# Optimization experiments

Hardware: AMD Instinct MI355X
Metric: run time of the kernel (lower is better)

The kernel has to match this reference:

```python
import jax, jax.numpy as jnp
import numpy as np

B, Cin, Cout, K, H, W = 16, 32, 32, 3, 256, 256
EMB = 256  # layer_pos_embedding_size == condition_size == 256


def setup_inputs() -> dict:
    key = jax.random.key(0)
    ks = jax.random.split(key, 7)
    return {
        "x": jax.random.normal(ks[0], (B, Cin, H, W), jnp.float32),
        "condition": jax.random.normal(ks[1], (B, EMB), jnp.float32),
        "layer_pos_embedding": jax.random.normal(ks[2], (B, EMB), jnp.float32),
        # base conv weight, stored [Cin, Cout, K, K] as in the torch module
        "weights": jax.random.normal(ks[3], (Cin, Cout, K, K), jnp.float32) * 0.05,
        "bias": jax.random.normal(ks[4], (Cout,), jnp.float32) * 0.05,
        # weightAdapt: Linear(2*EMB -> Cin); biasAdapt: Linear(2*EMB -> Cout)
        "wa_w": jax.random.normal(ks[5], (Cin, 2 * EMB), jnp.float32) * 0.04,
        "wa_b": jnp.zeros((Cin,), jnp.float32),
        "ba_w": jax.random.normal(ks[6], (Cout, 2 * EMB), jnp.float32) * 0.04,
        "ba_b": jnp.zeros((Cout,), jnp.float32),
    }


def reference(x, condition, layer_pos_embedding, weights, bias, wa_w, wa_b, ba_w, ba_b):
    # i = cat([condition, layer_pos_embedding])  -> [B, 2*EMB]
    i = jnp.concatenate([condition, layer_pos_embedding], axis=-1)
    wadapt = i @ wa_w.T + wa_b   # [B, Cin]  per-sample input-channel modulation
    badapt = i @ ba_w.T + ba_b   # [B, Cout] per-sample bias modulation
    # per-sample OIHW kernel: (weights [Cin,Cout,K,K] * wadapt[b,Cin,1,1,1]) rearranged
    kern = jnp.einsum('iokl,bi->boikl', weights, wadapt)  # [B, Cout, Cin, K, K]

    def conv1(xi, ki):
        # xi: [Cin,H,W], ki: [Cout,Cin,K,K] -> [Cout,H,W], padding='same', stride 1
        return jax.lax.conv_general_dilated(
            xi[None], ki, window_strides=(1, 1), padding='SAME',
            dimension_numbers=('NCHW', 'OIHW', 'NCHW'))[0]

    o = jax.vmap(conv1)(x, kern)  # [B, Cout, H, W] (== groups=batch grouped conv)
    # modulated bias add per (batch, out_channel)
    return o + (bias[None, :] * badapt)[:, :, None, None]
```

## Files before the change

### kernel.cpp

```cpp
#include <hip/hip_runtime.h>


#define B_    16
#define CIN   32
#define COUT  32
#define H_    256
#define W_    256
#define EMB2  512

#define XPX       66
#define PXS       32
#define ROWS_     (XPX*PXS)
#define NSLOT     8

using short8  = __attribute__((ext_vector_type(8))) short;
using float4v = __attribute__((ext_vector_type(4))) float;

__device__ __forceinline__ unsigned short f2bf(float f) {
    unsigned u = __builtin_bit_cast(unsigned, f);
    u += 0x7FFFu + ((u >> 16) & 1u);
    return (unsigned short)(u >> 16);
}
__device__ __forceinline__ unsigned pk2(float a, float b) {
    return (unsigned)f2bf(a) | ((unsigned)f2bf(b) << 16);
}

__global__ __launch_bounds__(256) void adapt_kernel(
    const float* __restrict__ cond, const float* __restrict__ lpe,
    const float* __restrict__ wa_w, const float* __restrict__ wa_b,
    const float* __restrict__ ba_w, const float* __restrict__ ba_b,
    const float* __restrict__ bias, float* __restrict__ ws)
{
    __shared__ float iv[EMB2];
    __shared__ float partial[64][4];
    const int b = blockIdx.x;
    const int t = threadIdx.x;

    iv[t]       = cond[b*256 + t];
    iv[t + 256] = lpe[b*256 + t];
    __syncthreads();

    const int out  = t & 63;
    const int part = t >> 6;
    const float* row = (out < 32) ? (wa_w + out*EMB2) : (ba_w + (out-32)*EMB2);
    float s = 0.f;
    #pragma unroll 8
    for (int j = part*128; j < part*128 + 128; ++j) s += iv[j] * row[j];
    partial[out][part] = s;
    __syncthreads();

    if (t < 64) {
        float v = partial[t][0] + partial[t][1] + partial[t][2] + partial[t][3];
        if (t < 32) ws[b*32 + t] = v + wa_b[t];
        else {
            int o = t - 32;
            ws[512 + b*32 + o] = bias[o] * (v + ba_b[o]);
        }
    }
}

__global__ __launch_bounds__(256, 2) void conv_kernel(
    const float* __restrict__ x, const float* __restrict__ weights,
    const float* __restrict__ ws, float* __restrict__ out)
{
    __shared__ unsigned short xbuf[NSLOT * ROWS_];
    __shared__ unsigned short wbuf[9 * COUT * PXS];

    const int tid    = threadIdx.x;
    const int lane   = tid & 63;
    const int w      = tid >> 6;
    const int ln15   = lane & 15;
    const int kg     = lane >> 4;
    const int xstrip = blockIdx.x * 64;
    const int ystrip = blockIdx.y * 32;
    const int b      = blockIdx.z;

    for (int idx = tid; idx < CIN*COUT*9; idx += 256) {
        int i   = idx / 288;
        int rem = idx - i*288;
        int o   = rem / 9;
        int tap = rem - o*9;
        float v = weights[idx] * ws[b*32 + i];
        wbuf[tap*1024 + o*32 + i] = f2bf(v);
    }

    auto stage = [&](int r0, int nrows) {
        const int total = nrows * XPX * 4;
        for (int idx = tid; idx < total; idx += 256) {
            int p  = idx % XPX;
            int t2 = idx / XPX;
            int g  = t2 & 3;
            int rr = t2 >> 2;
            int r  = r0 + rr;
            int gy = ystrip + r;
            int gx = xstrip + p - 1;
            int slot = (r + 1) & 7;
            unsigned dst = slot*ROWS_ + p*PXS + ((g ^ ((p >> 1) & 3)) * 8);
            uint4 pk;
            if (((unsigned)gy < 256u) & ((unsigned)gx < 256u)) {
                const float* src = x + (((size_t)(b*CIN + g*8) << 16) + (gy << 8) + gx);
                float f0 = src[0*65536], f1 = src[1*65536];
                float f2 = src[2*65536], f3 = src[3*65536];
                float f4 = src[4*65536], f5 = src[5*65536];
                float f6 = src[6*65536], f7 = src[7*65536];
                pk.x = pk2(f0, f1); pk.y = pk2(f2, f3);
                pk.z = pk2(f4, f5); pk.w = pk2(f6, f7);
            } else {
                pk = uint4{0u, 0u, 0u, 0u};
            }
            *(uint4*)&xbuf[dst] = pk;
        }
    };

    stage(-1, 6);
    __syncthreads();

    short8 wA[9][2];
    #pragma unroll
    for (int tap = 0; tap < 9; ++tap)
        #pragma unroll
        for (int ot = 0; ot < 2; ++ot) {
            int o = ot*16 + ln15;
            wA[tap][ot] = *(const short8*)&wbuf[tap*1024 + o*32 + kg*8];
        }

    float bm[2][4];
    #pragma unroll
    for (int ot = 0; ot < 2; ++ot)
        #pragma unroll
        for (int r = 0; r < 4; ++r)
            bm[ot][r] = ws[512 + b*32 + ot*16 + kg*4 + r];

    for (int t = 0; t < 8; ++t) {
        if (t > 0) {
            stage(4*t + 1, 4);
            __syncthreads();
        }

        const int orow = 4*t + w;
        const int gy   = ystrip + orow;

        float4v acc[4][2];
        #pragma unroll
        for (int c = 0; c < 4; ++c) {
            acc[c][0] = float4v{0.f, 0.f, 0.f, 0.f};
            acc[c][1] = float4v{0.f, 0.f, 0.f, 0.f};
        }

        #pragma unroll
        for (int dy = 0; dy < 3; ++dy) {
            const int rowbase = ((orow + dy) & 7) * ROWS_;
            #pragma unroll
            for (int dx = 0; dx < 3; ++dx) {
                const int tap = dy*3 + dx;
                #pragma unroll
                for (int c = 0; c < 4; ++c) {
                    int p = c*16 + dx + ln15;
                    int a = rowbase + p*PXS + ((kg ^ ((p >> 1) & 3)) * 8);
                    short8 xf = *(const short8*)&xbuf[a];
                    acc[c][0] = __builtin_amdgcn_mfma_f32_16x16x32_bf16(
                                    wA[tap][0], xf, acc[c][0], 0, 0, 0);
                    acc[c][1] = __builtin_amdgcn_mfma_f32_16x16x32_bf16(
                                    wA[tap][1], xf, acc[c][1], 0, 0, 0);
                }
            }
        }
        __syncthreads();

        #pragma unroll
        for (int c = 0; c < 4; ++c) {
            const int xcol = xstrip + c*16 + ln15;
            #pragma unroll
            for (int ot = 0; ot < 2; ++ot) {
                const int obase = ot*16 + kg*4;
                #pragma unroll
                for (int r = 0; r < 4; ++r) {
                    out[(((size_t)(b*COUT + obase + r) << 8) + gy << 8) + xcol] =
                        acc[c][ot][r] + bm[ot][r];
                }
            }
        }
    }
}

extern "C" void kernel_launch(void* const* d_in, const int* in_sizes, int n_in,
                              void* d_out, int out_size, void* d_ws, size_t ws_size,
                              hipStream_t stream) {
    const float* x       = (const float*)d_in[0];
    const float* cond    = (const float*)d_in[1];
    const float* lpe     = (const float*)d_in[2];
    const float* weights = (const float*)d_in[3];
    const float* bias    = (const float*)d_in[4];
    const float* wa_w    = (const float*)d_in[5];
    const float* wa_b    = (const float*)d_in[6];
    const float* ba_w    = (const float*)d_in[7];
    const float* ba_b    = (const float*)d_in[8];
    float* outp = (float*)d_out;
    float* ws   = (float*)d_ws;

    adapt_kernel<<<dim3(B_), dim3(256), 0, stream>>>(
        cond, lpe, wa_w, wa_b, ba_w, ba_b, bias, ws);

    conv_kernel<<<dim3(W_/64, H_/32, B_), dim3(256), 0, stream>>>(
        x, weights, ws, outp);
}
```

Measured before the change: 276.1 us.

## Use 512-thread blocks with register-prefetched row ring and LDS-resident weights

Doubles the conv block to 8 waves, each computing one output row per iteration, and widens the LDS row ring to 10 slots. The next 8 input rows are loaded into registers before compute and written to LDS after it, so global-load latency overlaps the MFMA work. Halo columns are staged separately. Per-tap weight fragments now live in LDS in a lane-ordered layout and are reloaded per tap instead of kept in registers. The tighter launch bound (512 threads, 4 blocks) caps VGPRs, so the 32-float prefetch buffer plus accumulators may spill.

Measured after the change: 311.6 us. 12.9% more time.

```diff
diff --git a/kernel.cpp b/kernel.cpp
--- a/kernel.cpp
+++ b/kernel.cpp
@@ -8,10 +8,10 @@
 #define W_    256
 #define EMB2  512
 
-#define XPX       66
-#define PXS       32
-#define ROWS_     (XPX*PXS)
-#define NSLOT     8
+#define XPX   66
+#define PXS   32
+#define ROWS_ (XPX*PXS)
+#define NSLOT 10
 
 using short8  = __attribute__((ext_vector_type(8))) short;
 using float4v = __attribute__((ext_vector_type(4))) float;
@@ -59,12 +59,12 @@
     }
 }
 
-__global__ __launch_bounds__(256, 2) void conv_kernel(
+__global__ __launch_bounds__(512, 4) void conv_kernel(
     const float* __restrict__ x, const float* __restrict__ weights,
     const float* __restrict__ ws, float* __restrict__ out)
 {
-    __shared__ unsigned short xbuf[NSLOT * ROWS_];
-    __shared__ unsigned short wbuf[9 * COUT * PXS];
+    __shared__ __align__(16) unsigned short xbuf[NSLOT * ROWS_];
+    __shared__ __align__(16) unsigned short wbuf[9 * 2 * 64 * 8];
 
     const int tid    = threadIdx.x;
     const int lane   = tid & 63;
@@ -75,54 +75,51 @@
     const int ystrip = blockIdx.y * 32;
     const int b      = blockIdx.z;
 
-    for (int idx = tid; idx < CIN*COUT*9; idx += 256) {
+    for (int idx = tid; idx < CIN*COUT*9; idx += 512) {
         int i   = idx / 288;
         int rem = idx - i*288;
         int o   = rem / 9;
         int tap = rem - o*9;
         float v = weights[idx] * ws[b*32 + i];
-        wbuf[tap*1024 + o*32 + i] = f2bf(v);
-    }
-
-    auto stage = [&](int r0, int nrows) {
-        const int total = nrows * XPX * 4;
-        for (int idx = tid; idx < total; idx += 256) {
-            int p  = idx % XPX;
-            int t2 = idx / XPX;
-            int g  = t2 & 3;
-            int rr = t2 >> 2;
-            int r  = r0 + rr;
-            int gy = ystrip + r;
-            int gx = xstrip + p - 1;
-            int slot = (r + 1) & 7;
-            unsigned dst = slot*ROWS_ + p*PXS + ((g ^ ((p >> 1) & 3)) * 8);
-            uint4 pk;
-            if (((unsigned)gy < 256u) & ((unsigned)gx < 256u)) {
-                const float* src = x + (((size_t)(b*CIN + g*8) << 16) + (gy << 8) + gx);
-                float f0 = src[0*65536], f1 = src[1*65536];
-                float f2 = src[2*65536], f3 = src[3*65536];
-                float f4 = src[4*65536], f5 = src[5*65536];
-                float f6 = src[6*65536], f7 = src[7*65536];
-                pk.x = pk2(f0, f1); pk.y = pk2(f2, f3);
-                pk.z = pk2(f4, f5); pk.w = pk2(f6, f7);
-            } else {
-                pk = uint4{0u, 0u, 0u, 0u};
-            }
-            *(uint4*)&xbuf[dst] = pk;
-        }
-    };
-
-    stage(-1, 6);
-    __syncthreads();
-
-    short8 wA[9][2];
+        wbuf[((tap*2 + (o>>4))*64 + ((i>>3)*16 + (o&15)))*8 + (i&7)] = f2bf(v);
+    }
+
+    auto load8 = [&](int g, int yy, int xx, float (&f)[8]) {
+        if (((unsigned)yy < 256u) & ((unsigned)xx < 256u)) {
+            const float* src = x + (((size_t)(b*CIN + g*8) << 16) + (yy << 8) + xx);
+            #pragma unroll
+            for (int j = 0; j < 8; ++j) f[j] = src[(size_t)j << 16];
+        } else {
+            #pragma unroll
+            for (int j = 0; j < 8; ++j) f[j] = 0.f;
+        }
+    };
+    auto packwrite = [&](int r, int p, int g, const float (&f)[8]) {
+        unsigned slot = (unsigned)(r + 1) % NSLOT;
+        unsigned dst  = slot*ROWS_ + p*PXS + ((g ^ ((p >> 1) & 3)) * 8);
+        uint4 pk;
+        pk.x = pk2(f[0], f[1]); pk.y = pk2(f[2], f[3]);
+        pk.z = pk2(f[4], f[5]); pk.w = pk2(f[6], f[7]);
+        *(uint4*)&xbuf[dst] = pk;
+    };
+
     #pragma unroll
-    for (int tap = 0; tap < 9; ++tap)
-        #pragma unroll
-        for (int ot = 0; ot < 2; ++ot) {
-            int o = ot*16 + ln15;
-            wA[tap][ot] = *(const short8*)&wbuf[tap*1024 + o*32 + kg*8];
-        }
+    for (int k = 0; k < 5; ++k) {
+        int ci = tid + k*512;
+        int pm = ci & 63, t2 = ci >> 6;
+        int g = t2 & 3, rr = t2 >> 2;
+        float f[8];
+        load8(g, ystrip + rr - 1, xstrip + pm, f);
+        packwrite(rr - 1, pm + 1, g, f);
+    }
+    if (tid < 80) {
+        int side = tid & 1, t2 = tid >> 1;
+        int g = t2 & 3, rr = t2 >> 2;
+        int p = side ? 65 : 0;
+        float f[8];
+        load8(g, ystrip + rr - 1, xstrip + p - 1, f);
+        packwrite(rr - 1, p, g, f);
+    }
 
     float bm[2][4];
     #pragma unroll
@@ -131,13 +128,44 @@
         for (int r = 0; r < 4; ++r)
             bm[ot][r] = ws[512 + b*32 + ot*16 + kg*4 + r];
 
-    for (int t = 0; t < 8; ++t) {
-        if (t > 0) {
-            stage(4*t + 1, 4);
-            __syncthreads();
-        }
-
-        const int orow = 4*t + w;
+    float P[4][8];
+    auto pf_issue = [&](int r0) {
+        #pragma unroll
+        for (int k = 0; k < 4; ++k) {
+            int ci = tid + k*512;
+            int pm = ci & 63, t2 = ci >> 6;
+            int g = t2 & 3, rr = t2 >> 2;
+            load8(g, ystrip + r0 + rr, xstrip + pm, P[k]);
+        }
+    };
+    auto pf_write = [&](int r0) {
+        #pragma unroll
+        for (int k = 0; k < 4; ++k) {
+            int ci = tid + k*512;
+            int pm = ci & 63, t2 = ci >> 6;
+            int g = t2 & 3, rr = t2 >> 2;
+            packwrite(r0 + rr, pm + 1, g, P[k]);
+        }
+    };
+    auto halo_stage = [&](int r0) {
+        if (tid < 64) {
+            int side = tid & 1, t2 = tid >> 1;
+            int g = t2 & 3, rr = t2 >> 2;
+            int p = side ? 65 : 0;
+            float f[8];
+            load8(g, ystrip + r0 + rr, xstrip + p - 1, f);
+            packwrite(r0 + rr, p, g, f);
+        }
+    };
+
+    pf_issue(9);
+
+    asm volatile("s_waitcnt lgkmcnt(0)" ::: "memory");
+    __builtin_amdgcn_s_barrier();
+    asm volatile("" ::: "memory");
+
+    for (int t = 0; t < 4; ++t) {
+        const int orow = 8*t + w;
         const int gy   = ystrip + orow;
 
         float4v acc[4][2];
@@ -149,22 +177,25 @@
 
         #pragma unroll
         for (int dy = 0; dy < 3; ++dy) {
-            const int rowbase = ((orow + dy) & 7) * ROWS_;
+            const int rowbase = (int)((unsigned)(orow + dy) % NSLOT) * ROWS_;
             #pragma unroll
             for (int dx = 0; dx < 3; ++dx) {
                 const int tap = dy*3 + dx;
+                short8 a0 = *(const short8*)&wbuf[((tap*2 + 0)*64 + lane)*8];
+                short8 a1 = *(const short8*)&wbuf[((tap*2 + 1)*64 + lane)*8];
                 #pragma unroll
                 for (int c = 0; c < 4; ++c) {
                     int p = c*16 + dx + ln15;
                     int a = rowbase + p*PXS + ((kg ^ ((p >> 1) & 3)) * 8);
                     short8 xf = *(const short8*)&xbuf[a];
                     acc[c][0] = __builtin_amdgcn_mfma_f32_16x16x32_bf16(
-                                    wA[tap][0], xf, acc[c][0], 0, 0, 0);
+                                    a0, xf, acc[c][0], 0, 0, 0);
                     acc[c][1] = __builtin_amdgcn_mfma_f32_16x16x32_bf16(
-                                    wA[tap][1], xf, acc[c][1], 0, 0, 0);
+                                    a1, xf, acc[c][1], 0, 0, 0);
                 }
             }
         }
+
         __syncthreads();
 
         #pragma unroll
@@ -175,10 +206,19 @@
                 const int obase = ot*16 + kg*4;
                 #pragma unroll
                 for (int r = 0; r < 4; ++r) {
-                    out[(((size_t)(b*COUT + obase + r) << 8) + gy << 8) + xcol] =
+                    out[((size_t)(b*COUT + obase + r)*256 + gy)*256 + xcol] =
                         acc[c][ot][r] + bm[ot][r];
                 }
             }
+        }
+
+        if (t < 3) {
+            halo_stage(8*t + 9);
+            pf_write(8*t + 9);
+            if (t < 2) pf_issue(8*t + 17);
+            asm volatile("s_waitcnt lgkmcnt(0)" ::: "memory");
+            __builtin_amdgcn_s_barrier();
+            asm volatile("" ::: "memory");
         }
     }
 }
@@ -201,6 +241,6 @@
     adapt_kernel<<<dim3(B_), dim3(256), 0, stream>>>(
         cond, lpe, wa_w, wa_b, ba_w, ba_b, bias, ws);
 
-    conv_kernel<<<dim3(W_/64, H_/32, B_), dim3(256), 0, stream>>>(
+    conv_kernel<<<dim3(W_/64, H_/32, B_), dim3(512), 0, stream>>>(
         x, weights, ws, outp);
 }
```
